# Performance work log

Hardware: AMD Instinct MI355X
Metric: run time of the kernel (lower is better)

The kernel has to match this reference:

```python
import jax, jax.numpy as jnp
import numpy as np


def setup_inputs() -> dict:
    key = jax.random.key(0)
    k1, k2, k3 = jax.random.split(key, 3)
    B, T, C = 16, 8192, 128  # batch, tokens, max_columns
    column_logits = jax.random.normal(k1, (B, T, C), dtype=jnp.float32)
    column_assignments = jax.random.randint(k2, (B, T), 0, C)
    valid_mask = jax.random.randint(k3, (B, T), 0, 2).astype(bool)
    return {
        "column_logits": column_logits,
        "column_assignments": column_assignments,
        "valid_mask": valid_mask,
    }


def reference(column_logits, column_assignments, valid_mask):
    # column_logits: (B, T, C); column_assignments: (B, T) int; valid_mask: (B, T) bool
    B, T, C = column_logits.shape
    probs = jax.nn.softmax(column_logits, axis=-1).reshape(-1, C)  # (N, C)
    seg = column_assignments.reshape(-1)                           # (N,)
    w = valid_mask.reshape(-1).astype(probs.dtype)                 # (N,)

    # Single-pass segmented stats over column ids (num_segments = max_columns).
    n = jax.ops.segment_sum(w, seg, num_segments=C)                       # (C,)
    s = jax.ops.segment_sum(probs * w[:, None], seg, num_segments=C)      # (C, C)
    n_safe = jnp.maximum(n, 1.0)
    mean = s / n_safe[:, None]                                            # per-column mean prob

    # Sum of squared deviations (matches torch's ((p - mean)**2).mean()).
    diff = probs - mean[seg]
    ssd = jax.ops.segment_sum((diff * diff) * w[:, None], seg, num_segments=C)  # (C, C)
    col_var = ssd.sum(axis=-1) / (n_safe * C)                                    # (C,)

    has_multi = n > 1.0  # columns with at least 2 valid tokens
    count = has_multi.sum().astype(col_var.dtype)
    total = jnp.where(has_multi, col_var, 0.0).sum()
    return jnp.where(count > 0, total / jnp.maximum(count, 1.0), 0.0)
```

## Files before the change

### kernel.cpp

```cpp
#include <hip/hip_runtime.h>
#include <hip/hip_bf16.h>


#define NROWS 131072
#define CC    128
#define NB    256

typedef float f32x16 __attribute__((ext_vector_type(16)));
typedef short bf16x8 __attribute__((ext_vector_type(8)));

union U4V { uint4 u; bf16x8 v; };
union H2U { __hip_bfloat162 h; unsigned int u; };


__global__ __launch_bounds__(1024) void k1_stats(
    const float* __restrict__ logits, const int* __restrict__ seg,
    const int* __restrict__ mask, ushort* __restrict__ Pm,
    float* __restrict__ slab_n, float* __restrict__ slab_q) {
  __shared__ int sm[512];
  __shared__ float n_lds[CC], q_lds[CC];
  const int t = threadIdx.x, b = blockIdx.x;
  if (t < CC) { n_lds[t] = 0.f; q_lds[t] = 0.f; }
  if (t < 512) {
    const int r = b * 512 + t;
    sm[t] = seg[r] | (mask[r] << 16);
  }
  __syncthreads();
  const int wave = t >> 6, lane = t & 63;
  const int q = lane >> 5, j5 = lane & 31;
#pragma unroll
  for (int g = 0; g < 2; ++g) {
    const int ts = 2 * wave + g;
    const int rb = ts * 16 + q * 8;
    float x[8][4];
#pragma unroll
    for (int i = 0; i < 8; ++i) {
      const float* rp = logits + (size_t)(b * 512 + rb + i) * CC + j5;
#pragma unroll
      for (int nt = 0; nt < 4; ++nt) x[i][nt] = rp[nt * 32];
    }
    float inv[8], qr[8];
#pragma unroll
    for (int i = 0; i < 8; ++i) {
      float z = 0.f, z2 = 0.f;
#pragma unroll
      for (int nt = 0; nt < 4; ++nt) {
        const float e = __expf(x[i][nt]);
        x[i][nt] = e; z += e; z2 += e * e;
      }
#pragma unroll
      for (int off = 1; off < 32; off <<= 1) {
        z  += __shfl_xor(z, off, 64);
        z2 += __shfl_xor(z2, off, 64);
      }
      inv[i] = 1.0f / z;
      qr[i] = z2 * inv[i] * inv[i];
    }
#pragma unroll
    for (int nt = 0; nt < 4; ++nt) {
      unsigned int d[4];
#pragma unroll
      for (int k = 0; k < 4; ++k) {
        H2U h;
        h.h = __float22bfloat162_rn(make_float2(
            x[2 * k][nt] * inv[2 * k], x[2 * k + 1][nt] * inv[2 * k + 1]));
        d[k] = h.u;
      }
      const size_t off16 =
          (((size_t)b * 128 + ts * 4 + nt) * 64 + lane) * 8;
      *(uint4*)(Pm + off16) = make_uint4(d[0], d[1], d[2], d[3]);
    }
    if (j5 == 0) {
#pragma unroll
      for (int i = 0; i < 8; ++i) {
        const int smv = sm[rb + i];
        if (smv >> 16) {
          atomicAdd(&n_lds[smv & 0xFFFF], 1.0f);
          atomicAdd(&q_lds[smv & 0xFFFF], qr[i]);
        }
      }
    }
  }
  __syncthreads();
  if (t < CC) {
    slab_n[t * NB + b] = n_lds[t];
    slab_q[t * NB + b] = q_lds[t];
  }
}

__global__ __launch_bounds__(256) void k2_gemm(
    const ushort* __restrict__ Pm, const int* __restrict__ seg,
    const int* __restrict__ mask, float* __restrict__ slab_s) {
  __shared__ unsigned int sg4[128];
  const int t = threadIdx.x, b = blockIdx.x;
  if (t < 128) {
    unsigned int w = 0;
#pragma unroll
    for (int k = 0; k < 4; ++k) {
      const int r = b * 512 + t * 4 + k;
      const unsigned int sv = mask[r] ? (unsigned int)seg[r] : 255u;
      w |= sv << (8 * k);
    }
    sg4[t] = w;
  }
  __syncthreads();
  const int wave = t >> 6, lane = t & 63;
  const int mm = wave * 32 + (lane & 31);
  const int q = lane >> 5;
  f32x16 acc0 = {}, acc1 = {}, acc2 = {}, acc3 = {};
  const ushort* pb = Pm + (size_t)b * 65536 + (size_t)lane * 8;
  for (int ks = 0; ks < 32; ++ks) {
    const unsigned int w0 = sg4[ks * 4 + q * 2];
    const unsigned int w1 = sg4[ks * 4 + q * 2 + 1];
    U4V a;
    {
      const unsigned int s0 = w0 & 255u, s1 = (w0 >> 8) & 255u;
      const unsigned int s2 = (w0 >> 16) & 255u, s3 = w0 >> 24;
      const unsigned int s4 = w1 & 255u, s5 = (w1 >> 8) & 255u;
      const unsigned int s6 = (w1 >> 16) & 255u, s7 = w1 >> 24;
      const unsigned int um = (unsigned int)mm;
      a.u = make_uint4(
          (s0 == um ? 0x3F80u : 0u) | (s1 == um ? 0x3F800000u : 0u),
          (s2 == um ? 0x3F80u : 0u) | (s3 == um ? 0x3F800000u : 0u),
          (s4 == um ? 0x3F80u : 0u) | (s5 == um ? 0x3F800000u : 0u),
          (s6 == um ? 0x3F80u : 0u) | (s7 == um ? 0x3F800000u : 0u));
    }
    U4V b0, b1, b2, b3;
    b0.u = *(const uint4*)(pb + (size_t)(ks * 4 + 0) * 512);
    b1.u = *(const uint4*)(pb + (size_t)(ks * 4 + 1) * 512);
    b2.u = *(const uint4*)(pb + (size_t)(ks * 4 + 2) * 512);
    b3.u = *(const uint4*)(pb + (size_t)(ks * 4 + 3) * 512);
    acc0 = __builtin_amdgcn_mfma_f32_32x32x16_bf16(a.v, b0.v, acc0, 0, 0, 0);
    acc1 = __builtin_amdgcn_mfma_f32_32x32x16_bf16(a.v, b1.v, acc1, 0, 0, 0);
    acc2 = __builtin_amdgcn_mfma_f32_32x32x16_bf16(a.v, b2.v, acc2, 0, 0, 0);
    acc3 = __builtin_amdgcn_mfma_f32_32x32x16_bf16(a.v, b3.v, acc3, 0, 0, 0);
  }
  float* out = slab_s + (size_t)b * (CC * CC);
  const int jcol = lane & 31;
  const int rbase = (lane >> 5) * 4;
#pragma unroll
  for (int reg = 0; reg < 16; ++reg) {
    const int c = wave * 32 + (reg & 3) + 8 * (reg >> 2) + rbase;
    out[c * CC + 0 * 32 + jcol] = acc0[reg];
    out[c * CC + 1 * 32 + jcol] = acc1[reg];
    out[c * CC + 2 * 32 + jcol] = acc2[reg];
    out[c * CC + 3 * 32 + jcol] = acc3[reg];
  }
}

__global__ __launch_bounds__(1024) void k3_colvar(
    const float* __restrict__ slab_s, const float* __restrict__ slab_n,
    const float* __restrict__ slab_q, float* __restrict__ colvar,
    float* __restrict__ flag) {
  const int c = blockIdx.x, t = threadIdx.x;
  const int j = t & 127, g8 = t >> 7;
  const float* base = slab_s + (size_t)g8 * (CC * CC) + (size_t)c * CC + j;
  float acc = 0.f;
#pragma unroll
  for (int i = 0; i < 32; ++i) acc += base[(size_t)(8 * i) * (CC * CC)];
  __shared__ float part[8 * CC];
  part[g8 * CC + j] = acc;
  __syncthreads();
  float tp = 0.f, np = 0.f, qp = 0.f;
  if (t < CC) {
    float s = 0.f;
#pragma unroll
    for (int g = 0; g < 8; ++g) s += part[g * CC + t];
    tp = s * s;
  } else if (t < 2 * CC) {
    const int k = t - CC;
    np = slab_n[c * NB + k] + slab_n[c * NB + k + 128];
  } else if (t < 3 * CC) {
    const int k = t - 2 * CC;
    qp = slab_q[c * NB + k] + slab_q[c * NB + k + 128];
  }
#pragma unroll
  for (int off = 32; off > 0; off >>= 1) {
    tp += __shfl_xor(tp, off, 64);
    np += __shfl_xor(np, off, 64);
    qp += __shfl_xor(qp, off, 64);
  }
  __shared__ float fin[3 * 16];
  if ((t & 63) == 0) {
    const int w = t >> 6;
    fin[w * 3 + 0] = tp; fin[w * 3 + 1] = np; fin[w * 3 + 2] = qp;
  }
  __syncthreads();
  if (t == 0) {
    float tt = 0.f, nn = 0.f, qq = 0.f;
#pragma unroll
    for (int i = 0; i < 16; ++i) {
      tt += fin[i * 3 + 0]; nn += fin[i * 3 + 1]; qq += fin[i * 3 + 2];
    }
    float cv = 0.f, fl = 0.f;
    if (nn > 1.0f) {
      cv = (qq - tt / nn) / (nn * (float)CC);
      fl = 1.f;
    }
    colvar[c] = cv;
    flag[c] = fl;
  }
}

__global__ __launch_bounds__(128) void final_k(
    const float* __restrict__ colvar, const float* __restrict__ flag,
    float* __restrict__ out) {
  const int j = threadIdx.x;
  float cv = colvar[j];
  float fl = flag[j];
#pragma unroll
  for (int off = 32; off > 0; off >>= 1) {
    cv += __shfl_xor(cv, off, 64);
    fl += __shfl_xor(fl, off, 64);
  }
  __shared__ float red[4];
  if ((j & 63) == 0) {
    const int w = j >> 6;
    red[w * 2 + 0] = cv;
    red[w * 2 + 1] = fl;
  }
  __syncthreads();
  if (j == 0) {
    const float total = red[0] + red[2];
    const float count = red[1] + red[3];
    out[0] = (count > 0.f) ? total / fmaxf(count, 1.f) : 0.f;
  }
}

__global__ __launch_bounds__(256) void rowstats_kernel(
    const float* __restrict__ logits, float2* __restrict__ stats) {
  const int wave = threadIdx.x >> 6;
  const int lane = threadIdx.x & 63;
  const int r = lane >> 2, cl = lane & 3;
  const int row = (blockIdx.x * 4 + wave) * 16 + r;
  const float4* rp = (const float4*)(logits + (size_t)row * CC);
  float z = 0.f, z2 = 0.f;
#pragma unroll
  for (int k = 0; k < 8; ++k) {
    const float4 x = rp[k * 4 + cl];
    const float e0 = __expf(x.x), e1 = __expf(x.y);
    const float e2 = __expf(x.z), e3 = __expf(x.w);
    z += (e0 + e1) + (e2 + e3);
    z2 += (e0 * e0 + e1 * e1) + (e2 * e2 + e3 * e3);
  }
  z += __shfl_xor(z, 1, 64);  z2 += __shfl_xor(z2, 1, 64);
  z += __shfl_xor(z, 2, 64);  z2 += __shfl_xor(z2, 2, 64);
  if (cl == 0) {
    const float inv = 1.0f / z;
    stats[row] = make_float2(inv, z2 * inv * inv);
  }
}

__global__ __launch_bounds__(1024) void scatter_kernel(
    const float* __restrict__ logits, const int* __restrict__ seg,
    const int* __restrict__ mask, const float2* __restrict__ stats,
    float* __restrict__ ws) {
  __shared__ float s_lds[CC * CC];
  __shared__ float n_lds[CC];
  __shared__ float q_lds[CC];
  for (int i = threadIdx.x; i < CC * CC; i += 1024) s_lds[i] = 0.f;
  if (threadIdx.x < CC) { n_lds[threadIdx.x] = 0.f; q_lds[threadIdx.x] = 0.f; }
  __syncthreads();
  const int wave = threadIdx.x >> 6;
  const int lane = threadIdx.x & 63;
  const int r = lane >> 2, cl = lane & 3;
  const int row0 = blockIdx.x * (NROWS / NB) + wave * 32;
#pragma unroll
  for (int it = 0; it < 2; ++it) {
    const int row = row0 + it * 16 + r;
    const int v = mask[row];
    const int c = seg[row];
    const float2 st = stats[row];
    if (v) {
      const float4* rp = (const float4*)(logits + (size_t)row * CC);
      const float inv = st.x;
      float* srow = s_lds + c * CC;
#pragma unroll
      for (int k = 0; k < 8; ++k) {
        const int kk = (k + r) & 7;
        const float4 x = rp[kk * 4 + cl];
        const int cb = kk * 16 + cl * 4;
        atomicAdd(&srow[cb + 0], __expf(x.x) * inv);
        atomicAdd(&srow[cb + 1], __expf(x.y) * inv);
        atomicAdd(&srow[cb + 2], __expf(x.z) * inv);
        atomicAdd(&srow[cb + 3], __expf(x.w) * inv);
      }
      if (cl == 0) {
        atomicAdd(&n_lds[c], 1.0f);
        atomicAdd(&q_lds[c], st.y);
      }
    }
  }
  __syncthreads();
  float4* dst = (float4*)(ws + (size_t)blockIdx.x * (CC * CC));
  const float4* src = (const float4*)s_lds;
  for (int i = threadIdx.x; i < CC * CC / 4; i += 1024) dst[i] = src[i];
  float* slab_n = ws + (size_t)NB * CC * CC;
  float* slab_q = slab_n + (size_t)CC * NB;
  if (threadIdx.x < CC) {
    slab_n[threadIdx.x * NB + blockIdx.x] = n_lds[threadIdx.x];
    slab_q[threadIdx.x * NB + blockIdx.x] = q_lds[threadIdx.x];
  }
}

__global__ __launch_bounds__(1024) void reduce_a(float* __restrict__ ws) {
  const int g = blockIdx.x >> 5;
  const int sl = blockIdx.x & 31;
  const int t = threadIdx.x;
  const int f4 = t & 127, kk = t >> 7;
  const float4* base =
      (const float4*)(ws + (size_t)(g * 32) * (CC * CC) + sl * 512);
  float4 acc = make_float4(0.f, 0.f, 0.f, 0.f);
#pragma unroll
  for (int i = 0; i < 4; ++i) {
    const float4 v = base[(size_t)(kk + 8 * i) * (CC * CC / 4) + f4];
    acc.x += v.x; acc.y += v.y; acc.z += v.z; acc.w += v.w;
  }
  __shared__ float4 part[8 * 128];
  part[kk * 128 + f4] = acc;
  __syncthreads();
  if (t < 128) {
    float4 s = part[t];
#pragma unroll
    for (int k = 1; k < 8; ++k) {
      const float4 v = part[k * 128 + t];
      s.x += v.x; s.y += v.y; s.z += v.z; s.w += v.w;
    }
    ((float4*)(ws + (size_t)(g * 32) * (CC * CC) + sl * 512))[t] = s;
  }
}

__global__ __launch_bounds__(1024) void reduce_b(
    const float* __restrict__ ws, float* __restrict__ colvar,
    float* __restrict__ flag) {
  const int c = blockIdx.x, t = threadIdx.x;
  __shared__ float p2[8 * 128];
  __shared__ float nb[256], qb[256];
  {
    const int g = t >> 7, j = t & 127;
    p2[g * 128 + j] = ws[(size_t)(g * 32) * (CC * CC) + (size_t)c * CC + j];
  }
  const float* slab_n = ws + (size_t)NB * CC * CC;
  const float* slab_q = slab_n + (size_t)CC * NB;
  if (t >= 256 && t < 512) nb[t - 256] = slab_n[c * NB + (t - 256)];
  else if (t >= 512 && t < 768) qb[t - 512] = slab_q[c * NB + (t - 512)];
  __syncthreads();
  if (t < 64) {
    float sa = 0.f, sb = 0.f;
#pragma unroll
    for (int g = 0; g < 8; ++g) {
      sa += p2[g * 128 + t];
      sb += p2[g * 128 + t + 64];
    }
    float tp = sa * sa + sb * sb;
    float np = nb[t] + nb[t + 64] + nb[t + 128] + nb[t + 192];
    float qp = qb[t] + qb[t + 64] + qb[t + 128] + qb[t + 192];
#pragma unroll
    for (int off = 1; off < 64; off <<= 1) {
      tp += __shfl_xor(tp, off, 64);
      np += __shfl_xor(np, off, 64);
      qp += __shfl_xor(qp, off, 64);
    }
    if (t == 0) {
      float cv = 0.f, fl = 0.f;
      if (np > 1.0f) {
        cv = (qp - tp / np) / (np * (float)CC);
        fl = 1.f;
      }
      colvar[c] = cv;
      flag[c] = fl;
    }
  }
}

extern "C" void kernel_launch(void* const* d_in, const int* in_sizes, int n_in,
                              void* d_out, int out_size, void* d_ws,
                              size_t ws_size, hipStream_t stream) {
  const float* logits = (const float*)d_in[0];
  const int* seg = (const int*)d_in[1];
  const int* mask = (const int*)d_in[2];
  float* out = (float*)d_out;

  const size_t MAIN_BYTES = 33554432ull + 16777216ull + 131072ull * 2 + 1024ull;
  if (ws_size >= MAIN_BYTES) {
    char* w8 = (char*)d_ws;
    ushort* Pm = (ushort*)w8;
    float* slab_s = (float*)(w8 + 33554432ull);
    float* slab_n = slab_s + 4194304;
    float* slab_q = slab_n + 32768;
    float* colvar = slab_q + 32768;
    float* flag = colvar + 128;
    k1_stats<<<NB, 1024, 0, stream>>>(logits, seg, mask, Pm, slab_n, slab_q);
    k2_gemm<<<NB, 256, 0, stream>>>(Pm, seg, mask, slab_s);
    k3_colvar<<<CC, 1024, 0, stream>>>(slab_s, slab_n, slab_q, colvar, flag);
    final_k<<<1, 128, 0, stream>>>(colvar, flag, out);
  } else {
    float* ws = (float*)d_ws;
    float* colvar = ws + (size_t)NB * CC * CC + 2 * (size_t)CC * NB;
    float* flag = colvar + CC;
    float2* stats = (float2*)(flag + CC);
    rowstats_kernel<<<NROWS / 64, 256, 0, stream>>>(logits, stats);
    scatter_kernel<<<NB, 1024, 0, stream>>>(logits, seg, mask, stats, ws);
    reduce_a<<<256, 1024, 0, stream>>>(ws);
    reduce_b<<<CC, 1024, 0, stream>>>(ws, colvar, flag);
    final_k<<<1, 128, 0, stream>>>(colvar, flag, out);
  }
}
```

Before: 122.6 us.

## Fuse softmax-stats and one-hot MFMA GEMM into one kernel via LDS

Merges the softmax/stats kernel and the one-hot bf16 MFMA segment-sum GEMM into a single kernel. The bf16 probability tile now stays in LDS (128 KB) instead of going out to and back from a 32 MB global buffer. This removes one launch and that global round trip. In exchange it uses heavy LDS per block, only 4 of 16 waves do the GEMM phase, and the fallback path for small workspaces is deleted.

Measured after the change: 109.0 us. 11.1% less time.

```diff
diff --git a/kernel.cpp b/kernel.cpp
--- a/kernel.cpp
+++ b/kernel.cpp
@@ -5,6 +5,7 @@
 #define NROWS 131072
 #define CC    128
 #define NB    256
+#define RPB   512
 
 typedef float f32x16 __attribute__((ext_vector_type(16)));
 typedef short bf16x8 __attribute__((ext_vector_type(8)));
@@ -12,20 +13,32 @@
 union U4V { uint4 u; bf16x8 v; };
 union H2U { __hip_bfloat162 h; unsigned int u; };
 
-
-__global__ __launch_bounds__(1024) void k1_stats(
+__global__ __launch_bounds__(1024) void fused_kernel(
     const float* __restrict__ logits, const int* __restrict__ seg,
-    const int* __restrict__ mask, ushort* __restrict__ Pm,
+    const int* __restrict__ mask, float* __restrict__ slab_s,
     float* __restrict__ slab_n, float* __restrict__ slab_q) {
-  __shared__ int sm[512];
+  __shared__ ushort Plds[RPB * CC];
+  __shared__ int sm[RPB];
+  __shared__ unsigned int sg4[128];
   __shared__ float n_lds[CC], q_lds[CC];
   const int t = threadIdx.x, b = blockIdx.x;
   if (t < CC) { n_lds[t] = 0.f; q_lds[t] = 0.f; }
-  if (t < 512) {
-    const int r = b * 512 + t;
+  if (t < RPB) {
+    const int r = b * RPB + t;
     sm[t] = seg[r] | (mask[r] << 16);
   }
   __syncthreads();
+  if (t < 128) {
+    unsigned int w = 0;
+#pragma unroll
+    for (int k = 0; k < 4; ++k) {
+      const int smv = sm[t * 4 + k];
+      const unsigned int sv = (smv >> 16) ? (unsigned int)(smv & 0xFFFF) : 255u;
+      w |= sv << (8 * k);
+    }
+    sg4[t] = w;
+  }
+
   const int wave = t >> 6, lane = t & 63;
   const int q = lane >> 5, j5 = lane & 31;
 #pragma unroll
@@ -35,7 +48,7 @@
     float x[8][4];
 #pragma unroll
     for (int i = 0; i < 8; ++i) {
-      const float* rp = logits + (size_t)(b * 512 + rb + i) * CC + j5;
+      const float* rp = logits + (size_t)(b * RPB + rb + i) * CC + j5;
 #pragma unroll
       for (int nt = 0; nt < 4; ++nt) x[i][nt] = rp[nt * 32];
     }
@@ -66,9 +79,8 @@
             x[2 * k][nt] * inv[2 * k], x[2 * k + 1][nt] * inv[2 * k + 1]));
         d[k] = h.u;
       }
-      const size_t off16 =
-          (((size_t)b * 128 + ts * 4 + nt) * 64 + lane) * 8;
-      *(uint4*)(Pm + off16) = make_uint4(d[0], d[1], d[2], d[3]);
+      *(uint4*)(Plds + ((size_t)(ts * 4 + nt) * 64 + lane) * 8) =
+          make_uint4(d[0], d[1], d[2], d[3]);
     }
     if (j5 == 0) {
 #pragma unroll
@@ -82,69 +94,51 @@
     }
   }
   __syncthreads();
-  if (t < CC) {
-    slab_n[t * NB + b] = n_lds[t];
-    slab_q[t * NB + b] = q_lds[t];
-  }
-}
-
-__global__ __launch_bounds__(256) void k2_gemm(
-    const ushort* __restrict__ Pm, const int* __restrict__ seg,
-    const int* __restrict__ mask, float* __restrict__ slab_s) {
-  __shared__ unsigned int sg4[128];
-  const int t = threadIdx.x, b = blockIdx.x;
-  if (t < 128) {
-    unsigned int w = 0;
-#pragma unroll
-    for (int k = 0; k < 4; ++k) {
-      const int r = b * 512 + t * 4 + k;
-      const unsigned int sv = mask[r] ? (unsigned int)seg[r] : 255u;
-      w |= sv << (8 * k);
-    }
-    sg4[t] = w;
-  }
-  __syncthreads();
-  const int wave = t >> 6, lane = t & 63;
-  const int mm = wave * 32 + (lane & 31);
-  const int q = lane >> 5;
-  f32x16 acc0 = {}, acc1 = {}, acc2 = {}, acc3 = {};
-  const ushort* pb = Pm + (size_t)b * 65536 + (size_t)lane * 8;
-  for (int ks = 0; ks < 32; ++ks) {
-    const unsigned int w0 = sg4[ks * 4 + q * 2];
-    const unsigned int w1 = sg4[ks * 4 + q * 2 + 1];
-    U4V a;
-    {
-      const unsigned int s0 = w0 & 255u, s1 = (w0 >> 8) & 255u;
-      const unsigned int s2 = (w0 >> 16) & 255u, s3 = w0 >> 24;
-      const unsigned int s4 = w1 & 255u, s5 = (w1 >> 8) & 255u;
-      const unsigned int s6 = (w1 >> 16) & 255u, s7 = w1 >> 24;
-      const unsigned int um = (unsigned int)mm;
-      a.u = make_uint4(
-          (s0 == um ? 0x3F80u : 0u) | (s1 == um ? 0x3F800000u : 0u),
-          (s2 == um ? 0x3F80u : 0u) | (s3 == um ? 0x3F800000u : 0u),
-          (s4 == um ? 0x3F80u : 0u) | (s5 == um ? 0x3F800000u : 0u),
-          (s6 == um ? 0x3F80u : 0u) | (s7 == um ? 0x3F800000u : 0u));
-    }
-    U4V b0, b1, b2, b3;
-    b0.u = *(const uint4*)(pb + (size_t)(ks * 4 + 0) * 512);
-    b1.u = *(const uint4*)(pb + (size_t)(ks * 4 + 1) * 512);
-    b2.u = *(const uint4*)(pb + (size_t)(ks * 4 + 2) * 512);
-    b3.u = *(const uint4*)(pb + (size_t)(ks * 4 + 3) * 512);
-    acc0 = __builtin_amdgcn_mfma_f32_32x32x16_bf16(a.v, b0.v, acc0, 0, 0, 0);
-    acc1 = __builtin_amdgcn_mfma_f32_32x32x16_bf16(a.v, b1.v, acc1, 0, 0, 0);
-    acc2 = __builtin_amdgcn_mfma_f32_32x32x16_bf16(a.v, b2.v, acc2, 0, 0, 0);
-    acc3 = __builtin_amdgcn_mfma_f32_32x32x16_bf16(a.v, b3.v, acc3, 0, 0, 0);
-  }
-  float* out = slab_s + (size_t)b * (CC * CC);
-  const int jcol = lane & 31;
-  const int rbase = (lane >> 5) * 4;
-#pragma unroll
-  for (int reg = 0; reg < 16; ++reg) {
-    const int c = wave * 32 + (reg & 3) + 8 * (reg >> 2) + rbase;
-    out[c * CC + 0 * 32 + jcol] = acc0[reg];
-    out[c * CC + 1 * 32 + jcol] = acc1[reg];
-    out[c * CC + 2 * 32 + jcol] = acc2[reg];
-    out[c * CC + 3 * 32 + jcol] = acc3[reg];
+
+  if (t >= 256 && t < 384) slab_n[(t - 256) * NB + b] = n_lds[t - 256];
+  else if (t >= 384 && t < 512) slab_q[(t - 384) * NB + b] = q_lds[t - 384];
+
+  if (wave < 4) {
+    const int mm = wave * 32 + (lane & 31);
+    f32x16 acc0 = {}, acc1 = {}, acc2 = {}, acc3 = {};
+    const ushort* pl = Plds + (size_t)lane * 8;
+    for (int ks = 0; ks < 32; ++ks) {
+      const unsigned int w0 = sg4[ks * 4 + q * 2];
+      const unsigned int w1 = sg4[ks * 4 + q * 2 + 1];
+      U4V a;
+      {
+        const unsigned int s0 = w0 & 255u, s1 = (w0 >> 8) & 255u;
+        const unsigned int s2 = (w0 >> 16) & 255u, s3 = w0 >> 24;
+        const unsigned int s4 = w1 & 255u, s5 = (w1 >> 8) & 255u;
+        const unsigned int s6 = (w1 >> 16) & 255u, s7 = w1 >> 24;
+        const unsigned int um = (unsigned int)mm;
+        a.u = make_uint4(
+            (s0 == um ? 0x3F80u : 0u) | (s1 == um ? 0x3F800000u : 0u),
+            (s2 == um ? 0x3F80u : 0u) | (s3 == um ? 0x3F800000u : 0u),
+            (s4 == um ? 0x3F80u : 0u) | (s5 == um ? 0x3F800000u : 0u),
+            (s6 == um ? 0x3F80u : 0u) | (s7 == um ? 0x3F800000u : 0u));
+      }
+      U4V b0, b1, b2, b3;
+      b0.u = *(const uint4*)(pl + (size_t)(ks * 4 + 0) * 512);
+      b1.u = *(const uint4*)(pl + (size_t)(ks * 4 + 1) * 512);
+      b2.u = *(const uint4*)(pl + (size_t)(ks * 4 + 2) * 512);
+      b3.u = *(const uint4*)(pl + (size_t)(ks * 4 + 3) * 512);
+      acc0 = __builtin_amdgcn_mfma_f32_32x32x16_bf16(a.v, b0.v, acc0, 0, 0, 0);
+      acc1 = __builtin_amdgcn_mfma_f32_32x32x16_bf16(a.v, b1.v, acc1, 0, 0, 0);
+      acc2 = __builtin_amdgcn_mfma_f32_32x32x16_bf16(a.v, b2.v, acc2, 0, 0, 0);
+      acc3 = __builtin_amdgcn_mfma_f32_32x32x16_bf16(a.v, b3.v, acc3, 0, 0, 0);
+    }
+    float* outp = slab_s + (size_t)b * (CC * CC);
+    const int jcol = lane & 31;
+    const int rbase = (lane >> 5) * 4;
+#pragma unroll
+    for (int reg = 0; reg < 16; ++reg) {
+      const int c = wave * 32 + (reg & 3) + 8 * (reg >> 2) + rbase;
+      outp[c * CC + 0 * 32 + jcol] = acc0[reg];
+      outp[c * CC + 1 * 32 + jcol] = acc1[reg];
+      outp[c * CC + 2 * 32 + jcol] = acc2[reg];
+      outp[c * CC + 3 * 32 + jcol] = acc3[reg];
+    }
   }
 }
 
@@ -227,152 +221,6 @@
   }
 }
 
-__global__ __launch_bounds__(256) void rowstats_kernel(
-    const float* __restrict__ logits, float2* __restrict__ stats) {
-  const int wave = threadIdx.x >> 6;
-  const int lane = threadIdx.x & 63;
-  const int r = lane >> 2, cl = lane & 3;
-  const int row = (blockIdx.x * 4 + wave) * 16 + r;
-  const float4* rp = (const float4*)(logits + (size_t)row * CC);
-  float z = 0.f, z2 = 0.f;
-#pragma unroll
-  for (int k = 0; k < 8; ++k) {
-    const float4 x = rp[k * 4 + cl];
-    const float e0 = __expf(x.x), e1 = __expf(x.y);
-    const float e2 = __expf(x.z), e3 = __expf(x.w);
-    z += (e0 + e1) + (e2 + e3);
-    z2 += (e0 * e0 + e1 * e1) + (e2 * e2 + e3 * e3);
-  }
-  z += __shfl_xor(z, 1, 64);  z2 += __shfl_xor(z2, 1, 64);
-  z += __shfl_xor(z, 2, 64);  z2 += __shfl_xor(z2, 2, 64);
-  if (cl == 0) {
-    const float inv = 1.0f / z;
-    stats[row] = make_float2(inv, z2 * inv * inv);
-  }
-}
-
-__global__ __launch_bounds__(1024) void scatter_kernel(
-    const float* __restrict__ logits, const int* __restrict__ seg,
-    const int* __restrict__ mask, const float2* __restrict__ stats,
-    float* __restrict__ ws) {
-  __shared__ float s_lds[CC * CC];
-  __shared__ float n_lds[CC];
-  __shared__ float q_lds[CC];
-  for (int i = threadIdx.x; i < CC * CC; i += 1024) s_lds[i] = 0.f;
-  if (threadIdx.x < CC) { n_lds[threadIdx.x] = 0.f; q_lds[threadIdx.x] = 0.f; }
-  __syncthreads();
-  const int wave = threadIdx.x >> 6;
-  const int lane = threadIdx.x & 63;
-  const int r = lane >> 2, cl = lane & 3;
-  const int row0 = blockIdx.x * (NROWS / NB) + wave * 32;
-#pragma unroll
-  for (int it = 0; it < 2; ++it) {
-    const int row = row0 + it * 16 + r;
-    const int v = mask[row];
-    const int c = seg[row];
-    const float2 st = stats[row];
-    if (v) {
-      const float4* rp = (const float4*)(logits + (size_t)row * CC);
-      const float inv = st.x;
-      float* srow = s_lds + c * CC;
-#pragma unroll
-      for (int k = 0; k < 8; ++k) {
-        const int kk = (k + r) & 7;
-        const float4 x = rp[kk * 4 + cl];
-        const int cb = kk * 16 + cl * 4;
-        atomicAdd(&srow[cb + 0], __expf(x.x) * inv);
-        atomicAdd(&srow[cb + 1], __expf(x.y) * inv);
-        atomicAdd(&srow[cb + 2], __expf(x.z) * inv);
-        atomicAdd(&srow[cb + 3], __expf(x.w) * inv);
-      }
-      if (cl == 0) {
-        atomicAdd(&n_lds[c], 1.0f);
-        atomicAdd(&q_lds[c], st.y);
-      }
-    }
-  }
-  __syncthreads();
-  float4* dst = (float4*)(ws + (size_t)blockIdx.x * (CC * CC));
-  const float4* src = (const float4*)s_lds;
-  for (int i = threadIdx.x; i < CC * CC / 4; i += 1024) dst[i] = src[i];
-  float* slab_n = ws + (size_t)NB * CC * CC;
-  float* slab_q = slab_n + (size_t)CC * NB;
-  if (threadIdx.x < CC) {
-    slab_n[threadIdx.x * NB + blockIdx.x] = n_lds[threadIdx.x];
-    slab_q[threadIdx.x * NB + blockIdx.x] = q_lds[threadIdx.x];
-  }
-}
-
-__global__ __launch_bounds__(1024) void reduce_a(float* __restrict__ ws) {
-  const int g = blockIdx.x >> 5;
-  const int sl = blockIdx.x & 31;
-  const int t = threadIdx.x;
-  const int f4 = t & 127, kk = t >> 7;
-  const float4* base =
-      (const float4*)(ws + (size_t)(g * 32) * (CC * CC) + sl * 512);
-  float4 acc = make_float4(0.f, 0.f, 0.f, 0.f);
-#pragma unroll
-  for (int i = 0; i < 4; ++i) {
-    const float4 v = base[(size_t)(kk + 8 * i) * (CC * CC / 4) + f4];
-    acc.x += v.x; acc.y += v.y; acc.z += v.z; acc.w += v.w;
-  }
-  __shared__ float4 part[8 * 128];
-  part[kk * 128 + f4] = acc;
-  __syncthreads();
-  if (t < 128) {
-    float4 s = part[t];
-#pragma unroll
-    for (int k = 1; k < 8; ++k) {
-      const float4 v = part[k * 128 + t];
-      s.x += v.x; s.y += v.y; s.z += v.z; s.w += v.w;
-    }
-    ((float4*)(ws + (size_t)(g * 32) * (CC * CC) + sl * 512))[t] = s;
-  }
-}
-
-__global__ __launch_bounds__(1024) void reduce_b(
-    const float* __restrict__ ws, float* __restrict__ colvar,
-    float* __restrict__ flag) {
-  const int c = blockIdx.x, t = threadIdx.x;
-  __shared__ float p2[8 * 128];
-  __shared__ float nb[256], qb[256];
-  {
-    const int g = t >> 7, j = t & 127;
-    p2[g * 128 + j] = ws[(size_t)(g * 32) * (CC * CC) + (size_t)c * CC + j];
-  }
-  const float* slab_n = ws + (size_t)NB * CC * CC;
-  const float* slab_q = slab_n + (size_t)CC * NB;
-  if (t >= 256 && t < 512) nb[t - 256] = slab_n[c * NB + (t - 256)];
-  else if (t >= 512 && t < 768) qb[t - 512] = slab_q[c * NB + (t - 512)];
-  __syncthreads();
-  if (t < 64) {
-    float sa = 0.f, sb = 0.f;
-#pragma unroll
-    for (int g = 0; g < 8; ++g) {
-      sa += p2[g * 128 + t];
-      sb += p2[g * 128 + t + 64];
-    }
-    float tp = sa * sa + sb * sb;
-    float np = nb[t] + nb[t + 64] + nb[t + 128] + nb[t + 192];
-    float qp = qb[t] + qb[t + 64] + qb[t + 128] + qb[t + 192];
-#pragma unroll
-    for (int off = 1; off < 64; off <<= 1) {
-      tp += __shfl_xor(tp, off, 64);
-      np += __shfl_xor(np, off, 64);
-      qp += __shfl_xor(qp, off, 64);
-    }
-    if (t == 0) {
-      float cv = 0.f, fl = 0.f;
-      if (np > 1.0f) {
-        cv = (qp - tp / np) / (np * (float)CC);
-        fl = 1.f;
-      }
-      colvar[c] = cv;
-      flag[c] = fl;
-    }
-  }
-}
-
 extern "C" void kernel_launch(void* const* d_in, const int* in_sizes, int n_in,
                               void* d_out, int out_size, void* d_ws,
                               size_t ws_size, hipStream_t stream) {
@@ -381,28 +229,13 @@
   const int* mask = (const int*)d_in[2];
   float* out = (float*)d_out;
 
-  const size_t MAIN_BYTES = 33554432ull + 16777216ull + 131072ull * 2 + 1024ull;
-  if (ws_size >= MAIN_BYTES) {
-    char* w8 = (char*)d_ws;
-    ushort* Pm = (ushort*)w8;
-    float* slab_s = (float*)(w8 + 33554432ull);
-    float* slab_n = slab_s + 4194304;
-    float* slab_q = slab_n + 32768;
-    float* colvar = slab_q + 32768;
-    float* flag = colvar + 128;
-    k1_stats<<<NB, 1024, 0, stream>>>(logits, seg, mask, Pm, slab_n, slab_q);
-    k2_gemm<<<NB, 256, 0, stream>>>(Pm, seg, mask, slab_s);
-    k3_colvar<<<CC, 1024, 0, stream>>>(slab_s, slab_n, slab_q, colvar, flag);
-    final_k<<<1, 128, 0, stream>>>(colvar, flag, out);
-  } else {
-    float* ws = (float*)d_ws;
-    float* colvar = ws + (size_t)NB * CC * CC + 2 * (size_t)CC * NB;
-    float* flag = colvar + CC;
-    float2* stats = (float2*)(flag + CC);
-    rowstats_kernel<<<NROWS / 64, 256, 0, stream>>>(logits, stats);
-    scatter_kernel<<<NB, 1024, 0, stream>>>(logits, seg, mask, stats, ws);
-    reduce_a<<<256, 1024, 0, stream>>>(ws);
-    reduce_b<<<CC, 1024, 0, stream>>>(ws, colvar, flag);
-    final_k<<<1, 128, 0, stream>>>(colvar, flag, out);
-  }
-}
+  float* slab_s = (float*)d_ws;
+  float* slab_n = slab_s + (size_t)NB * CC * CC;
+  float* slab_q = slab_n + CC * NB;
+  float* colvar = slab_q + CC * NB;
+  float* flag = colvar + CC;
+  fused_kernel<<<NB, 1024, 0, stream>>>(logits, seg, mask, slab_s, slab_n,
+                                        slab_q);
+  k3_colvar<<<CC, 1024, 0, stream>>>(slab_s, slab_n, slab_q, colvar, flag);
+  final_k<<<1, 128, 0, stream>>>(colvar, flag, out);
+}
```
